# Performance work log

Hardware: AMD Instinct MI355X
Metric: run time of the kernel (lower is better)

Reference implementation:

```python
import jax, jax.numpy as jnp
import numpy as np

HEADS = 8
MEM_LEN = 32


def _mha(q, k, v, Wq, bq, Wk, bk, Wv, bv, Wo, bo):
    # torch nn.MultiheadAttention, batch_first=False. q: [Lq,B,E], k/v: [Lk,B,E]
    Lq, B, E = q.shape
    d = E // HEADS

    def proj(t, W, b):
        p = t @ W.T + b
        return p.reshape(t.shape[0], B, HEADS, d).transpose(1, 2, 0, 3)  # [B,h,L,d]

    qh, kh, vh = proj(q, Wq, bq), proj(k, Wk, bk), proj(v, Wv, bv)
    scale = 1.0 / jnp.sqrt(jnp.asarray(d, q.dtype))
    att = jax.nn.softmax(jnp.einsum('bhqd,bhkd->bhqk', qh * scale, kh), axis=-1)
    out = jnp.einsum('bhqk,bhkd->bhqd', att, vh)          # [B,h,Lq,d]
    out = out.transpose(2, 0, 1, 3).reshape(Lq, B, E)
    return out @ Wo.T + bo


def _forward(x, h, c, memK, memV, externalK, externalV,
             W_ih, W_hh, b_ih, b_hh,
             sWq, sbq, sWk, sbk, sWv, sbv, sWo, sbo,
             cWq, cbq, cWk, cbk, cWv, cbv, cWo, cbo,
             Wres, bres, Wrout, brout, Wcomp, bcomp, Wexp, bexp, Wgate, bgate):
    H = h.shape[1]
    # LSTMCell (torch gate order i, f, g, o)
    gates = x @ W_ih.T + b_ih + h @ W_hh.T + b_hh
    i, f, g, o = jnp.split(gates, 4, axis=1)
    c_next = jax.nn.sigmoid(f) * c + jax.nn.sigmoid(i) * jnp.tanh(g)
    h_lstm = jax.nn.sigmoid(o) * jnp.tanh(c_next)
    # append detached h_lstm to short memory, keep last MEM_LEN entries
    cur = jax.lax.stop_gradient(h_lstm)[None]                      # [1,B,H]
    memK_new = jnp.concatenate([memK, cur], axis=0)[-MEM_LEN:]     # [ML,B,H]
    memV_new = jnp.concatenate([memV, cur], axis=0)[-MEM_LEN:]
    qSelf = h_lstm[None]                                           # [1,B,H]
    self_out = _mha(qSelf, memK_new, memV_new, sWq, sbq, sWk, sbk, sWv, sbv, sWo, sbo)[0]
    ext_out = _mha(qSelf, externalK, externalV, cWq, cbq, cWk, cbk, cWv, cbv, cWo, cbo)[0]
    rw = jax.nn.softmax(h_lstm @ Wrout.T + brout, axis=1)          # [B,2] router
    routed_attn = rw[:, :1] * self_out + rw[:, 1:2] * ext_out
    routed = h_lstm + routed_attn + routed_attn @ Wres.T + bres
    temporal_summary = memK_new.mean(axis=0)                       # [B,H]
    compressed = temporal_summary @ Wcomp.T + bcomp                # [B,H//4]
    expanded = compressed @ Wexp.T + bexp                          # [B,H]
    reps = -(-H // compressed.shape[1])
    compressed_expanded = jnp.tile(compressed, (1, reps))[:, :H]
    gate = jax.nn.sigmoid(jnp.concatenate([x, routed], axis=1) @ Wgate.T + bgate)
    hCT = compressed_expanded + gate * (expanded - compressed_expanded)  # torch.lerp
    hFinal = (h_lstm + routed + hCT) / 3.0                         # dropout = identity (eval)
    return hFinal, h_lstm, c_next


def setup_inputs() -> dict:
    key = jax.random.key(0)
    ks = jax.random.split(key, 34)
    B, I, H, ML, EL = 2048, 1024, 1024, 32, 32
    BN = H // 4
    rn = lambda k, s, sc=1.0: jax.random.normal(k, s, dtype=jnp.float32) * sc
    return {
        'x': rn(ks[0], (B, I)), 'h': rn(ks[1], (B, H)), 'c': rn(ks[2], (B, H)),
        'memK': rn(ks[3], (ML, B, H)), 'memV': rn(ks[4], (ML, B, H)),
        'externalK': rn(ks[5], (EL, B, H)), 'externalV': rn(ks[6], (EL, B, H)),
        'W_ih': rn(ks[7], (4 * H, I), 0.02), 'W_hh': rn(ks[8], (4 * H, H), 0.02),
        'b_ih': jnp.zeros((4 * H,), jnp.float32), 'b_hh': jnp.zeros((4 * H,), jnp.float32),
        'sWq': rn(ks[9], (H, H), 0.02), 'sbq': rn(ks[10], (H,), 0.02),
        'sWk': rn(ks[11], (H, H), 0.02), 'sbk': rn(ks[12], (H,), 0.02),
        'sWv': rn(ks[13], (H, H), 0.02), 'sbv': rn(ks[14], (H,), 0.02),
        'sWo': rn(ks[15], (H, H), 0.02), 'sbo': rn(ks[16], (H,), 0.02),
        'cWq': rn(ks[17], (H, H), 0.02), 'cbq': rn(ks[18], (H,), 0.02),
        'cWk': rn(ks[19], (H, H), 0.02), 'cbk': rn(ks[20], (H,), 0.02),
        'cWv': rn(ks[21], (H, H), 0.02), 'cbv': rn(ks[22], (H,), 0.02),
        'cWo': rn(ks[23], (H, H), 0.02), 'cbo': rn(ks[24], (H,), 0.02),
        'Wres': rn(ks[25], (H, H), 0.02), 'bres': rn(ks[26], (H,), 0.02),
        'Wrout': rn(ks[27], (2, H), 0.02), 'brout': rn(ks[28], (2,), 0.02),
        'Wcomp': rn(ks[29], (BN, H), 0.02), 'bcomp': rn(ks[30], (BN,), 0.02),
        'Wexp': rn(ks[31], (H, BN), 0.02), 'bexp': rn(ks[32], (H,), 0.02),
        'Wgate': rn(ks[33], (H, I + H), 0.02), 'bgate': jnp.zeros((H,), jnp.float32),
    }


def reference(x, h, c, memK, memV, externalK, externalV,
              W_ih, W_hh, b_ih, b_hh,
              sWq, sbq, sWk, sbk, sWv, sbv, sWo, sbo,
              cWq, cbq, cWk, cbk, cWv, cbv, cWo, cbo,
              Wres, bres, Wrout, brout, Wcomp, bcomp, Wexp, bexp, Wgate, bgate):
    return _forward(x, h, c, memK, memV, externalK, externalV,
                    W_ih, W_hh, b_ih, b_hh,
                    sWq, sbq, sWk, sbk, sWv, sbv, sWo, sbo,
                    cWq, cbq, cWk, cbk, cWv, cbv, cWo, cbo,
                    Wres, bres, Wrout, brout, Wcomp, bcomp, Wexp, bexp, Wgate, bgate)
```

## Files before the change

kernel.cpp:

```cpp
#include <hip/hip_runtime.h>
#include <math.h>

typedef __attribute__((ext_vector_type(4))) float f32x4;
typedef __attribute__((ext_vector_type(8))) short bf16x8;
typedef __attribute__((ext_vector_type(4))) unsigned short u16x4;
typedef __attribute__((ext_vector_type(8))) unsigned short u16x8;

__device__ __forceinline__ unsigned short f2bf(float f) {
  unsigned u = __builtin_bit_cast(unsigned, f);
  u += 0x7fffu + ((u >> 16) & 1u);
  return (unsigned short)(u >> 16);
}
__device__ __forceinline__ float bf2f(unsigned short s) {
  return __builtin_bit_cast(float, (unsigned)s << 16);
}
__device__ __forceinline__ float sigmoidf_(float x) { return 1.f / (1.f + __expf(-x)); }

struct CJob { const float* s; unsigned short* d; int nblk; };
struct CJobs { CJob j[14]; };

__global__ __launch_bounds__(256) void conv_k(CJobs jb) {
  int b = blockIdx.x;
  int i = 0;
  while (b >= jb.j[i].nblk) { b -= jb.j[i].nblk; ++i; }
  const long base = (long)b * 2048 + threadIdx.x * 8;
  f32x4 a = *(const f32x4*)(jb.j[i].s + base);
  f32x4 c = *(const f32x4*)(jb.j[i].s + base + 4);
  u16x8 o;
  o[0] = f2bf(a[0]); o[1] = f2bf(a[1]); o[2] = f2bf(a[2]); o[3] = f2bf(a[3]);
  o[4] = f2bf(c[0]); o[5] = f2bf(c[1]); o[6] = f2bf(c[2]); o[7] = f2bf(c[3]);
  *(u16x8*)(jb.j[i].d + base) = o;
}

template <int TN, int ACAT, int BCAT, int EPI, int ABF16, int BBF16, int OBF16>
__global__ __launch_bounds__(256) void gemm_k(
    const void* __restrict__ A1, const void* __restrict__ A1b, int lda1, long aZ,
    const void* __restrict__ A2, int lda2, int Ksplit,
    const void* __restrict__ B1, const void* __restrict__ B1b, int ldb1, long bZ,
    const void* __restrict__ B2, int ldb2,
    const float* __restrict__ bias1, const float* __restrict__ bias1b, long biasZ,
    const float* __restrict__ bias2,
    void* __restrict__ C, void* __restrict__ Cb, int ldc, long cZ,
    int K, int zs, float scale,
    const float* __restrict__ P0, const float* __restrict__ P1,
    const float* __restrict__ P2, const float* __restrict__ P3) {
  constexpr int NBI = TN / 32;
  __shared__ unsigned short As[2][128][32];
  __shared__ unsigned short Bs[2][TN][32];
  const int t = threadIdx.x;
  const int lane = t & 63;
  const int wave = t >> 6;
  const int wr = wave >> 1, wc = wave & 1;

  const unsigned gx = gridDim.x, gy = gridDim.y;
  unsigned L = blockIdx.x + gx * (blockIdx.y + gy * blockIdx.z);
  const unsigned nwg = gx * gy * gridDim.z;
  L = (L & 7u) * (nwg >> 3) + (L >> 3);
  const int bn = L % gx;
  const unsigned r1 = L / gx;
  const int bm = r1 % gy;
  const int z = r1 / gy;

  const bool hi = z >= zs;
  const int zz = hi ? z - zs : z;
  const char* Abase = (const char*)(hi ? A1b : A1) + (long)zz * aZ * (ABF16 ? 2 : 4);
  const char* Bbase = (const char*)(hi ? B1b : B1) + (long)zz * bZ * (BBF16 ? 2 : 4);
  const float* biasp = hi ? bias1b : bias1;
  char* Czc = (char*)(hi ? Cb : C) + (long)zz * cZ * (OBF16 ? 2 : 4);

  const int ar = t >> 3;
  const int bc = (t & 7) * 4;

  const int kIters = K >> 5;
  u16x4 Ra[4], Rb[NBI];

  auto loadT = [&](int kt) {
    const int k0 = kt << 5;
    const char* Ap; int ldA, kA;
    if (ACAT == 1 && k0 >= Ksplit) { Ap = (const char*)A2; ldA = lda2; kA = k0 - Ksplit; }
    else { Ap = Abase; ldA = lda1; kA = k0; }
    const char* Bp; int ldB, kB;
    if (BCAT == 1 && k0 >= Ksplit) { Bp = (const char*)B2; ldB = ldb2; kB = k0 - Ksplit; }
    else { Bp = Bbase; ldB = ldb1; kB = k0; }
#pragma unroll
    for (int i = 0; i < 4; ++i) {
      const long aoff = ((long)bm * 128 + ar + 32 * i) * ldA + kA + bc;
      if (ABF16) {
        Ra[i] = *(const u16x4*)((const unsigned short*)Ap + aoff);
      } else {
        f32x4 v = *(const f32x4*)((const float*)Ap + aoff);
        u16x4 pk;
        pk[0] = f2bf(v[0]); pk[1] = f2bf(v[1]); pk[2] = f2bf(v[2]); pk[3] = f2bf(v[3]);
        Ra[i] = pk;
      }
    }
#pragma unroll
    for (int i = 0; i < NBI; ++i) {
      const long boff = ((long)bn * TN + ar + 32 * i) * ldB + kB + bc;
      if (BBF16) {
        Rb[i] = *(const u16x4*)((const unsigned short*)Bp + boff);
      } else {
        f32x4 bv = *(const f32x4*)((const float*)Bp + boff);
        u16x4 bp;
        bp[0] = f2bf(bv[0]); bp[1] = f2bf(bv[1]); bp[2] = f2bf(bv[2]); bp[3] = f2bf(bv[3]);
        Rb[i] = bp;
      }
    }
  };

  loadT(0);

  f32x4 acc[4][NBI] = {};
  int p = 0;
  for (int kt = 0; kt < kIters; ++kt) {
    __syncthreads();
#pragma unroll
    for (int i = 0; i < 4; ++i) *(u16x4*)&As[p][ar + 32 * i][bc] = Ra[i];
#pragma unroll
    for (int i = 0; i < NBI; ++i) *(u16x4*)&Bs[p][ar + 32 * i][bc] = Rb[i];
    if (kt + 1 < kIters) loadT(kt + 1);
    __syncthreads();

    bf16x8 af[4], bfr[NBI];
#pragma unroll
    for (int mi = 0; mi < 4; ++mi)
      af[mi] = *(const bf16x8*)&As[p][wr * 64 + mi * 16 + (lane & 15)][(lane >> 4) * 8];
#pragma unroll
    for (int ni = 0; ni < NBI; ++ni)
      bfr[ni] = *(const bf16x8*)&Bs[p][wc * (TN / 2) + ni * 16 + (lane & 15)][(lane >> 4) * 8];
#pragma unroll
    for (int mi = 0; mi < 4; ++mi)
#pragma unroll
      for (int ni = 0; ni < NBI; ++ni)
        acc[mi][ni] = __builtin_amdgcn_mfma_f32_16x16x32_bf16(af[mi], bfr[ni], acc[mi][ni], 0, 0, 0);
    p ^= 1;
  }

  const int colb = bn * TN + wc * (TN / 2);
  const int rowb = bm * 128 + wr * 64;
#pragma unroll
  for (int mi = 0; mi < 4; ++mi) {
#pragma unroll
    for (int ni = 0; ni < NBI; ++ni) {
      f32x4 v = acc[mi][ni];
      const int col = colb + ni * 16 + (lane & 15);
      const int row0 = rowb + mi * 16 + ((lane >> 4) << 2);
      float bsum = 0.f;
      if (biasp) bsum += biasp[zz * biasZ + col];
      if (bias2) bsum += bias2[col];
#pragma unroll
      for (int q = 0; q < 4; ++q) {
        const long row = row0 + q;
        const long off = row * ldc + col;
        const float val = v[q] + bsum;
        if (EPI == 0) {
          if (OBF16) ((unsigned short*)Czc)[off] = f2bf(val * scale);
          else       ((float*)Czc)[off] = val * scale;
        } else if (EPI == 1) {
          const float r2 = val + P0[off] + P1[off];
          ((float*)Czc)[off] = r2;
          if (Cb) ((unsigned short*)Cb)[off] = f2bf(r2);
        } else if (EPI == 2) {
          const float g = sigmoidf_(val);
          const float ce = P0[row * 256 + (col & 255)];
          const float ex = P1[off];
          ((float*)Czc)[off] = (P2[off] + P3[off] + ce + g * (ex - ce)) * (1.f / 3.f);
        } else if (EPI == 3) {
          ((unsigned short*)Czc)[off] = f2bf(val * P0[2 * row + (hi ? 1 : 0)]);
        } else {
          ((float*)Czc)[off] = val + P2[2 * row] * P0[col] + P2[2 * row + 1] * P1[col];
        }
      }
    }
  }
}

__global__ __launch_bounds__(256) void transpose_k(const float* __restrict__ in0,
                                                   unsigned short* __restrict__ out0,
                                                   const float* __restrict__ in1,
                                                   unsigned short* __restrict__ out1, int n) {
  __shared__ float tile[64][65];
  const float* in = blockIdx.z ? in1 : in0;
  unsigned short* out = blockIdx.z ? out1 : out0;
  const int tr = blockIdx.y, tc = blockIdx.x, t = threadIdx.x;
#pragma unroll
  for (int it = 0; it < 16; ++it) {
    int idx = t + 256 * it;
    int r = idx >> 6, c = idx & 63;
    tile[r][c] = in[(long)(tr * 64 + r) * n + tc * 64 + c];
  }
  __syncthreads();
#pragma unroll
  for (int it = 0; it < 16; ++it) {
    int idx = t + 256 * it;
    int rr = idx >> 6, cc = idx & 63;
    out[(long)(tc * 64 + rr) * n + tr * 64 + cc] = f2bf(tile[cc][rr]);
  }
}

__global__ __launch_bounds__(256) void lstm_k(const float* __restrict__ gates,
                                              const float* __restrict__ c_in,
                                              const float* __restrict__ Wr,
                                              const float* __restrict__ br,
                                              float* __restrict__ c_out,
                                              float* __restrict__ h_ws,
                                              float* __restrict__ h_out,
                                              unsigned short* __restrict__ hlb,
                                              float* __restrict__ rw) {
  const int b = blockIdx.x, t = threadIdx.x;
  const long base = (long)b * 1024 + t * 4;
  const float* gb = gates + (long)b * 4096 + t * 4;
  f32x4 gi = *(const f32x4*)(gb);
  f32x4 gf = *(const f32x4*)(gb + 1024);
  f32x4 gg = *(const f32x4*)(gb + 2048);
  f32x4 go = *(const f32x4*)(gb + 3072);
  f32x4 cv = *(const f32x4*)(c_in + base);
  f32x4 cn, hv;
#pragma unroll
  for (int q = 0; q < 4; ++q) {
    float cc = sigmoidf_(gf[q]) * cv[q] + sigmoidf_(gi[q]) * tanhf(gg[q]);
    cn[q] = cc;
    hv[q] = sigmoidf_(go[q]) * tanhf(cc);
  }
  *(f32x4*)(c_out + base) = cn;
  *(f32x4*)(h_ws + base) = hv;
  *(f32x4*)(h_out + base) = hv;
  u16x4 hp;
  hp[0] = f2bf(hv[0]); hp[1] = f2bf(hv[1]); hp[2] = f2bf(hv[2]); hp[3] = f2bf(hv[3]);
  *(u16x4*)(hlb + base) = hp;
  f32x4 w0 = *(const f32x4*)(Wr + t * 4);
  f32x4 w1 = *(const f32x4*)(Wr + 1024 + t * 4);
  float a0 = hv[0] * w0[0] + hv[1] * w0[1] + hv[2] * w0[2] + hv[3] * w0[3];
  float a1 = hv[0] * w1[0] + hv[1] * w1[1] + hv[2] * w1[2] + hv[3] * w1[3];
#pragma unroll
  for (int m = 32; m >= 1; m >>= 1) {
    a0 += __shfl_xor(a0, m);
    a1 += __shfl_xor(a1, m);
  }
  __shared__ float red[8];
  if ((t & 63) == 0) { red[t >> 6] = a0; red[4 + (t >> 6)] = a1; }
  __syncthreads();
  if (t == 0) {
    float z0 = red[0] + red[1] + red[2] + red[3] + br[0];
    float z1 = red[4] + red[5] + red[6] + red[7] + br[1];
    float mx = fmaxf(z0, z1);
    float e0 = __expf(z0 - mx), e1 = __expf(z1 - mx);
    float s = e0 + e1;
    rw[2 * b] = e0 / s;
    rw[2 * b + 1] = e1 / s;
  }
}

__global__ __launch_bounds__(256) void attn10_k(
    const float* __restrict__ memK, const float* __restrict__ memV,
    const float* __restrict__ extK, const float* __restrict__ extV,
    const float* __restrict__ hl,
    const unsigned short* __restrict__ qtS, const unsigned short* __restrict__ qtE,
    unsigned short* __restrict__ mixS, unsigned short* __restrict__ mixE,
    float* __restrict__ ts) {
  const int NB = 2048, H = 1024;
  __shared__ float qtf[256 * 36];
  __shared__ float S_lds[32][8];
  __shared__ float P_lds[256];
  unsigned flat = blockIdx.x + gridDim.x * blockIdx.y;
  flat = (flat & 7u) * 512u + (flat >> 3);
  const int b = flat & 2047;
  const bool self = (flat >> 11) == 0;
  const int t = threadIdx.x;

  {
    const unsigned short* qtb = (self ? qtS : qtE) + (long)b * 8192;
#pragma unroll
    for (int i = 0; i < 4; ++i) {
      const int chunk = t + 256 * i;
      const int hh = chunk >> 7;
      const int pos = (chunk & 127) * 8;
      u16x8 qv = *(const u16x8*)(qtb + hh * 1024 + pos);
      const int kq0 = pos >> 2;
      f32x4 a, bb;
      a[0] = bf2f(qv[0]); a[1] = bf2f(qv[1]); a[2] = bf2f(qv[2]); a[3] = bf2f(qv[3]);
      bb[0] = bf2f(qv[4]); bb[1] = bf2f(qv[5]); bb[2] = bf2f(qv[6]); bb[3] = bf2f(qv[7]);
      *(f32x4*)&qtf[kq0 * 36 + hh * 4] = a;
      *(f32x4*)&qtf[(kq0 + 1) * 36 + hh * 4] = bb;
    }
  }
  __syncthreads();

  const int r = t >> 3, sub = t & 7;
  const float* Kr = self ? ((r < 31) ? memK + ((long)(r + 1) * NB + b) * H : hl + (long)b * H)
                         : extK + ((long)r * NB + b) * H;
  float acc[8] = {};
#pragma unroll
  for (int i = 0; i < 32; i += 4) {
    f32x4 kv[4];
#pragma unroll
    for (int u = 0; u < 4; ++u) kv[u] = *(const f32x4*)(Kr + ((i + u) * 8 + sub) * 4);
#pragma unroll
    for (int u = 0; u < 4; ++u) {
      const float* qp = &qtf[((i + u) * 8 + sub) * 36];
#pragma unroll
      for (int hh = 0; hh < 8; ++hh) {
        f32x4 q = *(const f32x4*)(qp + hh * 4);
        acc[hh] += kv[u][0] * q[0] + kv[u][1] * q[1] + kv[u][2] * q[2] + kv[u][3] * q[3];
      }
    }
  }
#pragma unroll
  for (int hh = 0; hh < 8; ++hh) {
    acc[hh] += __shfl_xor(acc[hh], 1);
    acc[hh] += __shfl_xor(acc[hh], 2);
    acc[hh] += __shfl_xor(acc[hh], 4);
  }
  if (sub == 0) {
#pragma unroll
    for (int hh = 0; hh < 8; ++hh) S_lds[r][hh] = acc[hh];
  }
  __syncthreads();

  {
    const int l = t & 31, hh = t >> 5;
    float Sv = S_lds[l][hh];
    float mx = Sv;
#pragma unroll
    for (int m = 16; m >= 1; m >>= 1) mx = fmaxf(mx, __shfl_xor(mx, m, 32));
    float pr = __expf(Sv - mx);
    float su = pr;
#pragma unroll
    for (int m = 16; m >= 1; m >>= 1) su += __shfl_xor(su, m, 32);
    P_lds[l * 8 + hh] = pr / su;
  }

  if (self) {
    const float* Kb = memK + (long)b * H + 4 * t;
    f32x4 a = {};
#pragma unroll
    for (int l = 0; l < 31; ++l) a += *(const f32x4*)(Kb + (long)(l + 1) * NB * H);
    a += *(const f32x4*)(hl + (long)b * H + 4 * t);
    *(f32x4*)(ts + (long)b * H + 4 * t) = a * (1.f / 32.f);
  }
  __syncthreads();

  const float* Vbase = (self ? memV + (long)NB * H : extV) + (long)b * H + 4 * t;
  const float* hlp = hl + (long)b * H + 4 * t;
  f32x4 vacc[8] = {};
#pragma unroll
  for (int l = 0; l < 32; l += 2) {
    f32x4 vv0 = *(const f32x4*)(Vbase + (long)l * NB * H);
    f32x4 vv1 = *(const f32x4*)((self && l + 1 == 31) ? hlp
                                                      : Vbase + (long)(l + 1) * NB * H);
    const float* Pl0 = &P_lds[l * 8];
    const float* Pl1 = &P_lds[(l + 1) * 8];
#pragma unroll
    for (int hh = 0; hh < 8; ++hh) vacc[hh] += Pl0[hh] * vv0;
#pragma unroll
    for (int hh = 0; hh < 8; ++hh) vacc[hh] += Pl1[hh] * vv1;
  }
  unsigned short* mixp = (self ? mixS : mixE) + (long)b * 8192;
#pragma unroll
  for (int hh = 0; hh < 8; ++hh) {
    u16x4 pk;
    pk[0] = f2bf(vacc[hh][0]); pk[1] = f2bf(vacc[hh][1]);
    pk[2] = f2bf(vacc[hh][2]); pk[3] = f2bf(vacc[hh][3]);
    *(u16x4*)(mixp + hh * 1024 + 4 * t) = pk;
  }
}

extern "C" void kernel_launch(void* const* d_in, const int* in_sizes, int n_in,
                              void* d_out, int out_size, void* d_ws, size_t ws_size,
                              hipStream_t stream) {
  const float* x    = (const float*)d_in[0];
  const float* h    = (const float*)d_in[1];
  const float* c    = (const float*)d_in[2];
  const float* memK = (const float*)d_in[3];
  const float* memV = (const float*)d_in[4];
  const float* extK = (const float*)d_in[5];
  const float* extV = (const float*)d_in[6];
  const float* W_ih = (const float*)d_in[7];
  const float* W_hh = (const float*)d_in[8];
  const float* b_ih = (const float*)d_in[9];
  const float* b_hh = (const float*)d_in[10];
  const float* sWq = (const float*)d_in[11];
  const float* sbq = (const float*)d_in[12];
  const float* sWk = (const float*)d_in[13];
  const float* sWv = (const float*)d_in[15];
  const float* sbv = (const float*)d_in[16];
  const float* sWo = (const float*)d_in[17];
  const float* sbo = (const float*)d_in[18];
  const float* cWq = (const float*)d_in[19];
  const float* cbq = (const float*)d_in[20];
  const float* cWk = (const float*)d_in[21];
  const float* cWv = (const float*)d_in[23];
  const float* cbv = (const float*)d_in[24];
  const float* cWo = (const float*)d_in[25];
  const float* cbo = (const float*)d_in[26];
  const float* Wres = (const float*)d_in[27];
  const float* bres = (const float*)d_in[28];
  const float* Wrout = (const float*)d_in[29];
  const float* brout = (const float*)d_in[30];
  const float* Wcomp = (const float*)d_in[31];
  const float* bcomp = (const float*)d_in[32];
  const float* Wexp = (const float*)d_in[33];
  const float* bexp = (const float*)d_in[34];
  const float* Wgate = (const float*)d_in[35];
  const float* bgate = (const float*)d_in[36];
  (void)in_sizes; (void)n_in; (void)out_size; (void)ws_size;

  float* out = (float*)d_out;
  float* w = (float*)d_ws;
  const long M1 = 1024 * 1024;
  const long U = 1024 * 1024;
  unsigned short* ub = (unsigned short*)w;

  float* gates   = w;
  float* hl      = w + 8 * M1;
  unsigned short* qsS = (unsigned short*)(w + 10 * M1);
  unsigned short* qsE = (unsigned short*)(w + 12 * M1);
  unsigned short* qtS = (unsigned short*)(w + 16 * M1);
  unsigned short* qtE = (unsigned short*)(w + 32 * M1);
  unsigned short* mixS = (unsigned short*)(w + 48 * M1);
  unsigned short* mixE = (unsigned short*)(w + 64 * M1);
  float* ts      = w + 80 * M1;
  unsigned short* attnS = (unsigned short*)(w + 82 * M1);
  unsigned short* attnE = (unsigned short*)(w + 84 * M1);
  float* rw      = w + 90 * M1;
  float* rattn   = w + 91 * M1;
  float* routed  = w + 93 * M1;
  float* comp    = w + 95 * M1;
  float* expd    = w + 96 * M1;

  unsigned short* Wihb  = ub + 48 * U;
  unsigned short* Whhb  = ub + 52 * U;
  unsigned short* xb    = ub + 56 * U;
  unsigned short* hb    = ub + 58 * U;
  unsigned short* sWqb  = ub + 60 * U;
  unsigned short* cWqb  = ub + 61 * U;
  unsigned short* sWvb  = ub + 62 * U;
  unsigned short* cWvb  = ub + 63 * U;
  unsigned short* sWob  = ub + 80 * U;
  unsigned short* cWob  = ub + 81 * U;
  unsigned short* Wresb = ub + 82 * U;
  unsigned short* Wcompb= ub + 83 * U;
  unsigned short* Wexpb = ub + 84 * U;
  unsigned short* Wgateb= ub + 85 * U;
  unsigned short* wkTsb = ub + 87 * U;
  unsigned short* wkTcb = ub + 88 * U;
  unsigned short* hlb   = ub + 89 * U;
  unsigned short* routedb = ub + 91 * U;

  float* hFinal_out = out;
  float* hl_out     = out + 2 * M1;
  float* cn_out     = out + 4 * M1;

  const float scaleq = 0.08838834764831845f;
  const int ZBIG = 1 << 30;
  dim3 blk(256);
  const float* nf = nullptr;
  const void* nv = nullptr;

  CJobs jb;
  jb.j[0] = {x, xb, 1024};
  jb.j[1] = {h, hb, 1024};
  jb.j[2] = {W_ih, Wihb, 2048};
  jb.j[3] = {W_hh, Whhb, 2048};
  jb.j[4] = {sWq, sWqb, 512};
  jb.j[5] = {cWq, cWqb, 512};
  jb.j[6] = {sWv, sWvb, 512};
  jb.j[7] = {cWv, cWvb, 512};
  jb.j[8] = {sWo, sWob, 512};
  jb.j[9] = {cWo, cWob, 512};
  jb.j[10] = {Wres, Wresb, 512};
  jb.j[11] = {Wcomp, Wcompb, 128};
  jb.j[12] = {Wexp, Wexpb, 128};
  jb.j[13] = {Wgate, Wgateb, 1024};
  conv_k<<<11008, blk, 0, stream>>>(jb);

  transpose_k<<<dim3(16, 16, 2), blk, 0, stream>>>(sWk, wkTsb, cWk, wkTcb, 1024);

  gemm_k<128, 1, 1, 0, 1, 1, 0><<<dim3(32, 16, 1), blk, 0, stream>>>(
      xb, nv, 1024, 0, hb, 1024, 1024,
      Wihb, nv, 1024, 0, Whhb, 1024,
      b_ih, nf, 0, b_hh,
      gates, nullptr, 4096, 0,
      2048, ZBIG, 1.f, nf, nf, nf, nf);

  lstm_k<<<2048, blk, 0, stream>>>(gates, c, Wrout, brout, cn_out, hl, hl_out, hlb, rw);

  gemm_k<128, 0, 0, 0, 1, 1, 1><<<dim3(8, 16, 2), blk, 0, stream>>>(
      hlb, hlb, 1024, 0, nv, 0, 0,
      sWqb, cWqb, 1024, 0, nv, 0,
      sbq, cbq, 0, nf,
      qsS, qsE, 1024, 0,
      1024, 1, scaleq, nf, nf, nf, nf);

  gemm_k<128, 0, 0, 0, 1, 1, 1><<<dim3(8, 16, 16), blk, 0, stream>>>(
      qsS, qsE, 1024, 128, nv, 0, 0,
      wkTsb, wkTcb, 1024, 128, nv, 0,
      nf, nf, 0, nf,
      qtS, qtE, 8192, 1024,
      128, 8, 1.f, nf, nf, nf, nf);

  attn10_k<<<dim3(2048, 2), blk, 0, stream>>>(memK, memV, extK, extV, hl,
                                              qtS, qtE, mixS, mixE, ts);

  gemm_k<64, 0, 0, 3, 1, 1, 1><<<dim3(2, 16, 16), blk, 0, stream>>>(
      mixS, mixE, 8192, 1024, nv, 0, 0,
      sWvb, cWvb, 1024, 131072, nv, 0,
      sbv, cbv, 128, nf,
      attnS, attnE, 1024, 128,
      1024, 8, 1.f, rw, nf, nf, nf);

  gemm_k<64, 1, 1, 4, 1, 1, 0><<<dim3(16, 16, 1), blk, 0, stream>>>(
      attnS, nv, 1024, 0, attnE, 1024, 1024,
      sWob, nv, 1024, 0, cWob, 1024,
      nf, nf, 0, nf,
      rattn, nullptr, 1024, 0,
      2048, ZBIG, 1.f, sbo, cbo, rw, nf);

  gemm_k<64, 0, 0, 1, 0, 1, 0><<<dim3(16, 16, 1), blk, 0, stream>>>(
      rattn, nv, 1024, 0, nv, 0, 0,
      Wresb, nv, 1024, 0, nv, 0,
      bres, nf, 0, nf,
      routed, routedb, 1024, 0,
      1024, ZBIG, 1.f, hl, rattn, nf, nf);

  gemm_k<64, 0, 0, 0, 0, 1, 0><<<dim3(4, 16, 1), blk, 0, stream>>>(
      ts, nv, 1024, 0, nv, 0, 0,
      Wcompb, nv, 1024, 0, nv, 0,
      bcomp, nf, 0, nf,
      comp, nullptr, 256, 0,
      1024, ZBIG, 1.f, nf, nf, nf, nf);
  gemm_k<64, 0, 0, 0, 0, 1, 0><<<dim3(16, 16, 1), blk, 0, stream>>>(
      comp, nv, 256, 0, nv, 0, 0,
      Wexpb, nv, 256, 0, nv, 0,
      bexp, nf, 0, nf,
      expd, nullptr, 1024, 0,
      256, ZBIG, 1.f, nf, nf, nf, nf);

  gemm_k<64, 1, 0, 2, 1, 1, 0><<<dim3(16, 16, 1), blk, 0, stream>>>(
      xb, nv, 1024, 0, routedb, 1024, 1024,
      Wgateb, nv, 2048, 0, nv, 0,
      bgate, nf, 0, nf,
      hFinal_out, nullptr, 1024, 0,
      2048, ZBIG, 1.f, comp, expd, hl, routed);
}
```

Measured before the change: 659.7 us.

## Load bf16 GEMM tiles directly into LDS with global_load_lds, split fp32 path

Adds a new gemm2_k for all-bf16 operands that uses the global_load_lds builtin to copy tiles straight from global memory into shared memory. This skips the register round-trip and uses a single LDS buffer instead of register-prefetch double buffering. The fp32-input GEMMs (Wres residual, compress, expand) stay on a simplified gemm_k. The risk is that, with one buffer and a sync right after the loads, global latency is no longer overlapped with the MFMA compute.

```diff
diff --git a/kernel.cpp b/kernel.cpp
--- a/kernel.cpp
+++ b/kernel.cpp
@@ -32,12 +32,14 @@
   *(u16x8*)(jb.j[i].d + base) = o;
 }
 
-template <int TN, int ACAT, int BCAT, int EPI, int ABF16, int BBF16, int OBF16>
-__global__ __launch_bounds__(256) void gemm_k(
-    const void* __restrict__ A1, const void* __restrict__ A1b, int lda1, long aZ,
-    const void* __restrict__ A2, int lda2, int Ksplit,
-    const void* __restrict__ B1, const void* __restrict__ B1b, int ldb1, long bZ,
-    const void* __restrict__ B2, int ldb2,
+template <int TN, int ACAT, int BCAT, int EPI, int OBF16>
+__global__ __launch_bounds__(256) void gemm2_k(
+    const unsigned short* __restrict__ A1, const unsigned short* __restrict__ A1b,
+    int lda1, long aZ,
+    const unsigned short* __restrict__ A2, int lda2, int Ksplit,
+    const unsigned short* __restrict__ B1, const unsigned short* __restrict__ B1b,
+    int ldb1, long bZ,
+    const unsigned short* __restrict__ B2, int ldb2,
     const float* __restrict__ bias1, const float* __restrict__ bias1b, long biasZ,
     const float* __restrict__ bias2,
     void* __restrict__ C, void* __restrict__ Cb, int ldc, long cZ,
@@ -45,8 +47,8 @@
     const float* __restrict__ P0, const float* __restrict__ P1,
     const float* __restrict__ P2, const float* __restrict__ P3) {
   constexpr int NBI = TN / 32;
-  __shared__ unsigned short As[2][128][32];
-  __shared__ unsigned short Bs[2][TN][32];
+  __shared__ unsigned short As[128][32];
+  __shared__ unsigned short Bs[TN][32];
   const int t = threadIdx.x;
   const int lane = t & 63;
   const int wave = t >> 6;
@@ -63,77 +65,54 @@
 
   const bool hi = z >= zs;
   const int zz = hi ? z - zs : z;
-  const char* Abase = (const char*)(hi ? A1b : A1) + (long)zz * aZ * (ABF16 ? 2 : 4);
-  const char* Bbase = (const char*)(hi ? B1b : B1) + (long)zz * bZ * (BBF16 ? 2 : 4);
+  const unsigned short* Abase = (hi ? A1b : A1) + (long)zz * aZ;
+  const unsigned short* Bbase = (hi ? B1b : B1) + (long)zz * bZ;
   const float* biasp = hi ? bias1b : bias1;
   char* Czc = (char*)(hi ? Cb : C) + (long)zz * cZ * (OBF16 ? 2 : 4);
 
-  const int ar = t >> 3;
-  const int bc = (t & 7) * 4;
+  const int rowT = t >> 2;
+  const int segT = (t & 3) * 8;
 
   const int kIters = K >> 5;
-  u16x4 Ra[4], Rb[NBI];
-
-  auto loadT = [&](int kt) {
+  f32x4 acc[4][NBI] = {};
+  for (int kt = 0; kt < kIters; ++kt) {
     const int k0 = kt << 5;
-    const char* Ap; int ldA, kA;
-    if (ACAT == 1 && k0 >= Ksplit) { Ap = (const char*)A2; ldA = lda2; kA = k0 - Ksplit; }
+    const unsigned short* Ap; int ldA, kA;
+    if (ACAT == 1 && k0 >= Ksplit) { Ap = A2; ldA = lda2; kA = k0 - Ksplit; }
     else { Ap = Abase; ldA = lda1; kA = k0; }
-    const char* Bp; int ldB, kB;
-    if (BCAT == 1 && k0 >= Ksplit) { Bp = (const char*)B2; ldB = ldb2; kB = k0 - Ksplit; }
+    const unsigned short* Bp; int ldB, kB;
+    if (BCAT == 1 && k0 >= Ksplit) { Bp = B2; ldB = ldb2; kB = k0 - Ksplit; }
     else { Bp = Bbase; ldB = ldb1; kB = k0; }
-#pragma unroll
-    for (int i = 0; i < 4; ++i) {
-      const long aoff = ((long)bm * 128 + ar + 32 * i) * ldA + kA + bc;
-      if (ABF16) {
-        Ra[i] = *(const u16x4*)((const unsigned short*)Ap + aoff);
-      } else {
-        f32x4 v = *(const f32x4*)((const float*)Ap + aoff);
-        u16x4 pk;
-        pk[0] = f2bf(v[0]); pk[1] = f2bf(v[1]); pk[2] = f2bf(v[2]); pk[3] = f2bf(v[3]);
-        Ra[i] = pk;
-      }
-    }
-#pragma unroll
-    for (int i = 0; i < NBI; ++i) {
-      const long boff = ((long)bn * TN + ar + 32 * i) * ldB + kB + bc;
-      if (BBF16) {
-        Rb[i] = *(const u16x4*)((const unsigned short*)Bp + boff);
-      } else {
-        f32x4 bv = *(const f32x4*)((const float*)Bp + boff);
-        u16x4 bp;
-        bp[0] = f2bf(bv[0]); bp[1] = f2bf(bv[1]); bp[2] = f2bf(bv[2]); bp[3] = f2bf(bv[3]);
-        Rb[i] = bp;
-      }
-    }
-  };
-
-  loadT(0);
-
-  f32x4 acc[4][NBI] = {};
-  int p = 0;
-  for (int kt = 0; kt < kIters; ++kt) {
+
     __syncthreads();
 #pragma unroll
-    for (int i = 0; i < 4; ++i) *(u16x4*)&As[p][ar + 32 * i][bc] = Ra[i];
-#pragma unroll
-    for (int i = 0; i < NBI; ++i) *(u16x4*)&Bs[p][ar + 32 * i][bc] = Rb[i];
-    if (kt + 1 < kIters) loadT(kt + 1);
+    for (int i = 0; i < 2; ++i) {
+      const unsigned short* g = Ap + ((long)bm * 128 + rowT + 64 * i) * ldA + kA + segT;
+      __builtin_amdgcn_global_load_lds(
+          (const __attribute__((address_space(1))) void*)g,
+          (__attribute__((address_space(3))) void*)&As[rowT + 64 * i][segT], 16, 0, 0);
+    }
+#pragma unroll
+    for (int i = 0; i < TN / 64; ++i) {
+      const unsigned short* g = Bp + ((long)bn * TN + rowT + 64 * i) * ldB + kB + segT;
+      __builtin_amdgcn_global_load_lds(
+          (const __attribute__((address_space(1))) void*)g,
+          (__attribute__((address_space(3))) void*)&Bs[rowT + 64 * i][segT], 16, 0, 0);
+    }
     __syncthreads();
 
     bf16x8 af[4], bfr[NBI];
 #pragma unroll
     for (int mi = 0; mi < 4; ++mi)
-      af[mi] = *(const bf16x8*)&As[p][wr * 64 + mi * 16 + (lane & 15)][(lane >> 4) * 8];
+      af[mi] = *(const bf16x8*)&As[wr * 64 + mi * 16 + (lane & 15)][(lane >> 4) * 8];
 #pragma unroll
     for (int ni = 0; ni < NBI; ++ni)
-      bfr[ni] = *(const bf16x8*)&Bs[p][wc * (TN / 2) + ni * 16 + (lane & 15)][(lane >> 4) * 8];
+      bfr[ni] = *(const bf16x8*)&Bs[wc * (TN / 2) + ni * 16 + (lane & 15)][(lane >> 4) * 8];
 #pragma unroll
     for (int mi = 0; mi < 4; ++mi)
 #pragma unroll
       for (int ni = 0; ni < NBI; ++ni)
         acc[mi][ni] = __builtin_amdgcn_mfma_f32_16x16x32_bf16(af[mi], bfr[ni], acc[mi][ni], 0, 0, 0);
-    p ^= 1;
   }
 
   const int colb = bn * TN + wc * (TN / 2);
@@ -156,10 +135,6 @@
         if (EPI == 0) {
           if (OBF16) ((unsigned short*)Czc)[off] = f2bf(val * scale);
           else       ((float*)Czc)[off] = val * scale;
-        } else if (EPI == 1) {
-          const float r2 = val + P0[off] + P1[off];
-          ((float*)Czc)[off] = r2;
-          if (Cb) ((unsigned short*)Cb)[off] = f2bf(r2);
         } else if (EPI == 2) {
           const float g = sigmoidf_(val);
           const float ce = P0[row * 256 + (col & 255)];
@@ -167,8 +142,122 @@
           ((float*)Czc)[off] = (P2[off] + P3[off] + ce + g * (ex - ce)) * (1.f / 3.f);
         } else if (EPI == 3) {
           ((unsigned short*)Czc)[off] = f2bf(val * P0[2 * row + (hi ? 1 : 0)]);
+        } else if (EPI == 4) {
+          ((float*)Czc)[off] = val + P2[2 * row] * P0[col] + P2[2 * row + 1] * P1[col];
+        }
+      }
+    }
+  }
+}
+
+template <int TN, int EPI, int ABF16, int BBF16, int OBF16>
+__global__ __launch_bounds__(256) void gemm_k(
+    const void* __restrict__ A1, int lda1,
+    const void* __restrict__ B1, int ldb1,
+    const float* __restrict__ bias1,
+    void* __restrict__ C, void* __restrict__ Cb, int ldc,
+    int K, float scale,
+    const float* __restrict__ P0, const float* __restrict__ P1) {
+  constexpr int NBI = TN / 32;
+  __shared__ unsigned short As[2][128][32];
+  __shared__ unsigned short Bs[2][TN][32];
+  const int t = threadIdx.x;
+  const int lane = t & 63;
+  const int wave = t >> 6;
+  const int wr = wave >> 1, wc = wave & 1;
+
+  const unsigned gx = gridDim.x, gy = gridDim.y;
+  unsigned L = blockIdx.x + gx * blockIdx.y;
+  const unsigned nwg = gx * gy;
+  L = (L & 7u) * (nwg >> 3) + (L >> 3);
+  const int bn = L % gx;
+  const int bm = L / gx;
+
+  const int ar = t >> 3;
+  const int bc = (t & 7) * 4;
+
+  const int kIters = K >> 5;
+  u16x4 Ra[4], Rb[NBI];
+
+  auto loadT = [&](int kt) {
+    const int k0 = kt << 5;
+#pragma unroll
+    for (int i = 0; i < 4; ++i) {
+      const long aoff = ((long)bm * 128 + ar + 32 * i) * lda1 + k0 + bc;
+      if (ABF16) {
+        Ra[i] = *(const u16x4*)((const unsigned short*)A1 + aoff);
+      } else {
+        f32x4 v = *(const f32x4*)((const float*)A1 + aoff);
+        u16x4 pk;
+        pk[0] = f2bf(v[0]); pk[1] = f2bf(v[1]); pk[2] = f2bf(v[2]); pk[3] = f2bf(v[3]);
+        Ra[i] = pk;
+      }
+    }
+#pragma unroll
+    for (int i = 0; i < NBI; ++i) {
+      const long boff = ((long)bn * TN + ar + 32 * i) * ldb1 + k0 + bc;
+      if (BBF16) {
+        Rb[i] = *(const u16x4*)((const unsigned short*)B1 + boff);
+      } else {
+        f32x4 bv = *(const f32x4*)((const float*)B1 + boff);
+        u16x4 bp;
+        bp[0] = f2bf(bv[0]); bp[1] = f2bf(bv[1]); bp[2] = f2bf(bv[2]); bp[3] = f2bf(bv[3]);
+        Rb[i] = bp;
+      }
+    }
+  };
+
+  loadT(0);
+
+  f32x4 acc[4][NBI] = {};
+  int p = 0;
+  for (int kt = 0; kt < kIters; ++kt) {
+    __syncthreads();
+#pragma unroll
+    for (int i = 0; i < 4; ++i) *(u16x4*)&As[p][ar + 32 * i][bc] = Ra[i];
+#pragma unroll
+    for (int i = 0; i < NBI; ++i) *(u16x4*)&Bs[p][ar + 32 * i][bc] = Rb[i];
+    if (kt + 1 < kIters) loadT(kt + 1);
+    __syncthreads();
+
+    bf16x8 af[4], bfr[NBI];
+#pragma unroll
+    for (int mi = 0; mi < 4; ++mi)
+      af[mi] = *(const bf16x8*)&As[p][wr * 64 + mi * 16 + (lane & 15)][(lane >> 4) * 8];
+#pragma unroll
+    for (int ni = 0; ni < NBI; ++ni)
+      bfr[ni] = *(const bf16x8*)&Bs[p][wc * (TN / 2) + ni * 16 + (lane & 15)][(lane >> 4) * 8];
+#pragma unroll
+    for (int mi = 0; mi < 4; ++mi)
+#pragma unroll
+      for (int ni = 0; ni < NBI; ++ni)
+        acc[mi][ni] = __builtin_amdgcn_mfma_f32_16x16x32_bf16(af[mi], bfr[ni], acc[mi][ni], 0, 0, 0);
+    p ^= 1;
+  }
+
+  const int colb = bn * TN + wc * (TN / 2);
+  const int rowb = bm * 128 + wr * 64;
+#pragma unroll
+  for (int mi = 0; mi < 4; ++mi) {
+#pragma unroll
+    for (int ni = 0; ni < NBI; ++ni) {
+      f32x4 v = acc[mi][ni];
+      const int col = colb + ni * 16 + (lane & 15);
+      const int row0 = rowb + mi * 16 + ((lane >> 4) << 2);
+      float bsum = 0.f;
+      if (bias1) bsum += bias1[col];
+#pragma unroll
+      for (int q = 0; q < 4; ++q) {
+        const long row = row0 + q;
+        const long off = row * ldc + col;
+        const float val = v[q] + bsum;
+        if (EPI == 0) {
+          if (OBF16) ((unsigned short*)C)[off] = f2bf(val * scale);
+          else       ((float*)C)[off] = val * scale;
         } else {
-          ((float*)Czc)[off] = val + P2[2 * row] * P0[col] + P2[2 * row + 1] * P1[col];
+          const float r2 = val + P0[off] + P1[off];
+          ((float*)C)[off] = r2;
+          if (Cb) ((unsigned short*)Cb)[off] = f2bf(r2);
         }
       }
     }
@@ -455,7 +544,7 @@
   const int ZBIG = 1 << 30;
   dim3 blk(256);
   const float* nf = nullptr;
-  const void* nv = nullptr;
+  const unsigned short* nu = nullptr;
 
   CJobs jb;
   jb.j[0] = {x, xb, 1024};
@@ -476,25 +565,25 @@
 
   transpose_k<<<dim3(16, 16, 2), blk, 0, stream>>>(sWk, wkTsb, cWk, wkTcb, 1024);
 
-  gemm_k<128, 1, 1, 0, 1, 1, 0><<<dim3(32, 16, 1), blk, 0, stream>>>(
-      xb, nv, 1024, 0, hb, 1024, 1024,
-      Wihb, nv, 1024, 0, Whhb, 1024,
+  gemm2_k<128, 1, 1, 0, 0><<<dim3(32, 16, 1), blk, 0, stream>>>(
+      xb, nu, 1024, 0, hb, 1024, 1024,
+      Wihb, nu, 1024, 0, Whhb, 1024,
       b_ih, nf, 0, b_hh,
       gates, nullptr, 4096, 0,
       2048, ZBIG, 1.f, nf, nf, nf, nf);
 
   lstm_k<<<2048, blk, 0, stream>>>(gates, c, Wrout, brout, cn_out, hl, hl_out, hlb, rw);
 
-  gemm_k<128, 0, 0, 0, 1, 1, 1><<<dim3(8, 16, 2), blk, 0, stream>>>(
-      hlb, hlb, 1024, 0, nv, 0, 0,
-      sWqb, cWqb, 1024, 0, nv, 0,
+  gemm2_k<128, 0, 0, 0, 1><<<dim3(8, 16, 2), blk, 0, stream>>>(
+      hlb, hlb, 1024, 0, nu, 0, 0,
+      sWqb, cWqb, 1024, 0, nu, 0,
       sbq, cbq, 0, nf,
       qsS, qsE, 1024, 0,
       1024, 1, scaleq, nf, nf, nf, nf);
 
-  gemm_k<128, 0, 0, 0, 1, 1, 1><<<dim3(8, 16, 16), blk, 0, stream>>>(
-      qsS, qsE, 1024, 128, nv, 0, 0,
-      wkTsb, wkTcb, 1024, 128, nv, 0,
+  gemm2_k<128, 0, 0, 0, 1><<<dim3(8, 16, 16), blk, 0, stream>>>(
+      qsS, qsE, 1024, 128, nu, 0, 0,
+      wkTsb, wkTcb, 1024, 128, nu, 0,
       nf, nf, 0, nf,
       qtS, qtE, 8192, 1024,
       128, 8, 1.f, nf, nf, nf, nf);
@@ -502,43 +591,37 @@
   attn10_k<<<dim3(2048, 2), blk, 0, stream>>>(memK, memV, extK, extV, hl,
                                               qtS, qtE, mixS, mixE, ts);
 
-  gemm_k<64, 0, 0, 3, 1, 1, 1><<<dim3(2, 16, 16), blk, 0, stream>>>(
-      mixS, mixE, 8192, 1024, nv, 0, 0,
-      sWvb, cWvb, 1024, 131072, nv, 0,
+  gemm2_k<64, 0, 0, 3, 1><<<dim3(2, 16, 16), blk, 0, stream>>>(
+      mixS, mixE, 8192, 1024, nu, 0, 0,
+      sWvb, cWvb, 1024, 131072, nu, 0,
       sbv, cbv, 128, nf,
       attnS, attnE, 1024, 128,
       1024, 8, 1.f, rw, nf, nf, nf);
 
-  gemm_k<64, 1, 1, 4, 1, 1, 0><<<dim3(16, 16, 1), blk, 0, stream>>>(
-      attnS, nv, 1024, 0, attnE, 1024, 1024,
-      sWob, nv, 1024, 0, cWob, 1024,
+  gemm2_k<64, 1, 1, 4, 0><<<dim3(16, 16, 1), blk, 0, stream>>>(
+      attnS, nu, 1024, 0, attnE, 1024, 1024,
+      sWob, nu, 1024, 0, cWob, 1024,
       nf, nf, 0, nf,
       rattn, nullptr, 1024, 0,
       2048, ZBIG, 1.f, sbo, cbo, rw, nf);
 
-  gemm_k<64, 0, 0, 1, 0, 1, 0><<<dim3(16, 16, 1), blk, 0, stream>>>(
-      rattn, nv, 1024, 0, nv, 0, 0,
-      Wresb, nv, 1024, 0, nv, 0,
-      bres, nf, 0, nf,
-      routed, routedb, 1024, 0,
-      1024, ZBIG, 1.f, hl, rattn, nf, nf);
-
-  gemm_k<64, 0, 0, 0, 0, 1, 0><<<dim3(4, 16, 1), blk, 0, stream>>>(
-      ts, nv, 1024, 0, nv, 0, 0,
-      Wcompb, nv, 1024, 0, nv, 0,
-      bcomp, nf, 0, nf,
-      comp, nullptr, 256, 0,
-      1024, ZBIG, 1.f, nf, nf, nf, nf);
-  gemm_k<64, 0, 0, 0, 0, 1, 0><<<dim3(16, 16, 1), blk, 0, stream>>>(
-      comp, nv, 256, 0, nv, 0, 0,
-      Wexpb, nv, 256, 0, nv, 0,
-      bexp, nf, 0, nf,
-      expd, nullptr, 1024, 0,
-      256, ZBIG, 1.f, nf, nf, nf, nf);
-
-  gemm_k<64, 1, 0, 2, 1, 1, 0><<<dim3(16, 16, 1), blk, 0, stream>>>(
-      xb, nv, 1024, 0, routedb, 1024, 1024,
-      Wgateb, nv, 2048, 0, nv, 0,
+  gemm_k<64, 1, 0, 1, 0><<<dim3(16, 16), blk, 0, stream>>>(
+      rattn, 1024, Wresb, 1024, bres,
+      routed, routedb, 1024,
+      1024, 1.f, hl, rattn);
+
+  gemm_k<64, 0, 0, 1, 0><<<dim3(4, 16), blk, 0, stream>>>(
+      ts, 1024, Wcompb, 1024, bcomp,
+      comp, nullptr, 256,
+      1024, 1.f, nf, nf);
+  gemm_k<64, 0, 0, 1, 0><<<dim3(16, 16), blk, 0, stream>>>(
+      comp, 256, Wexpb, 256, bexp,
+      expd, nullptr, 1024,
+      256, 1.f, nf, nf);
+
+  gemm2_k<64, 1, 0, 2, 0><<<dim3(16, 16, 1), blk, 0, stream>>>(
+      xb, nu, 1024, 0, routedb, 1024, 1024,
+      Wgateb, nu, 2048, 0, nu, 0,
       bgate, nf, 0, nf,
       hFinal_out, nullptr, 1024, 0,
       2048, ZBIG, 1.f, comp, expd, hl, routed);
```

New measurement: 673.2 us. 1.02x slower.
